# Kernel tuning notes

Hardware: AMD Instinct MI355X
Metric: run time of the kernel (lower is better)

## Reference

```python
import jax, jax.numpy as jnp
import numpy as np

D = 1024
H = 8
HD = D // H
SCALE = HD ** -0.5


def setup_inputs() -> dict:
    key = jax.random.key(0)
    ks = jax.random.split(key, 12)
    s = 0.02
    return {
        "x": jax.random.normal(ks[0], (4, 2048, D), dtype=jnp.float32),
        "attn_mask": jax.random.randint(ks[1], (2048, 2048), 0, 2, dtype=jnp.int32),
        "qkv_w": jax.random.normal(ks[2], (3 * D, D), dtype=jnp.float32) * s,
        "qkv_b": jnp.zeros((3 * D,), dtype=jnp.float32),
        "q_w": jax.random.normal(ks[3], (D, D), dtype=jnp.float32) * s,
        "q_b": jnp.zeros((D,), dtype=jnp.float32),
        "k_w": jax.random.normal(ks[4], (D, D), dtype=jnp.float32) * s,
        "k_b": jnp.zeros((D,), dtype=jnp.float32),
        "v_w": jax.random.normal(ks[5], (D, D), dtype=jnp.float32) * s,
        "v_b": jnp.zeros((D,), dtype=jnp.float32),
        "out_w": jax.random.normal(ks[6], (D, D), dtype=jnp.float32) * s,
        "out_b": jnp.zeros((D,), dtype=jnp.float32),
    }


def reference(x, attn_mask, qkv_w, qkv_b, q_w, q_b, k_w, k_b, v_w, v_b, out_w, out_b):
    B, S, _ = x.shape
    qkv = x @ qkv_w.T + qkv_b
    q, k, v = jnp.split(qkv, 3, axis=-1)
    # per-stream multi-head projections, then split heads: [B,H,S,HD]
    def heads(t, w, b):
        return (t @ w.T + b).reshape(B, S, H, HD).transpose(0, 2, 1, 3)
    q = heads(q, q_w, q_b)
    k = heads(k, k_w, k_b)
    v = heads(v, v_w, v_b)
    # scaled dot-product attention with masked softmax
    scores = jnp.einsum("bhqd,bhkd->bhqk", q, k) * SCALE
    scores = jnp.where(attn_mask == 1, -jnp.inf, scores)
    attn = jax.nn.softmax(scores, axis=-1)
    o = jnp.einsum("bhqk,bhkd->bhqd", attn, v)
    o = o.transpose(0, 2, 1, 3).reshape(B, S, D)
    return o @ out_w.T + out_b
```

## Files before the change

kernel.cpp:

```cpp
#include <hip/hip_runtime.h>
#include <stdint.h>

typedef unsigned short u16;
typedef unsigned int u32;
typedef unsigned long long u64;
using f32x4 = __attribute__((ext_vector_type(4))) float;
using s16x8 = __attribute__((ext_vector_type(8))) short;
using u16x4 = __attribute__((ext_vector_type(4))) unsigned short;

static constexpr float kQScale = (float)(0.08838834764831845 * 1.4426950408889634);

__device__ __forceinline__ u16 f2bf(float f) {
  uint32_t u = __float_as_uint(f);
  u += 0x7fffu + ((u >> 16) & 1u);
  return (u16)(u >> 16);
}

__device__ __forceinline__ float fexp2(float x) {
#if __has_builtin(__builtin_amdgcn_exp2f)
  return __builtin_amdgcn_exp2f(x);
#else
  return exp2f(x);
#endif
}

__device__ __forceinline__ void mfma16(f32x4& d, s16x8 a, s16x8 b) {
  asm volatile("v_mfma_f32_16x16x32_bf16 %0, %1, %2, %0" : "+v"(d) : "v"(a), "v"(b));
}
__device__ __forceinline__ f32x4 mfma16_z(s16x8 a, s16x8 b) {
  f32x4 d;
  asm volatile("v_mfma_f32_16x16x32_bf16 %0, %1, %2, 0" : "=&v"(d) : "v"(a), "v"(b));
  return d;
}

__device__ __forceinline__ void g2lds16(const void* g, void* l) {
  __builtin_amdgcn_global_load_lds(
      (__attribute__((address_space(1))) void*)(uintptr_t)g,
      (__attribute__((address_space(3))) void*)(uint32_t)(uintptr_t)l, 16, 0, 0);
}

__global__ __launch_bounds__(256) void cvt_f32_bf16(const float* __restrict__ in,
                                                    u16* __restrict__ out, int n) {
  int i = (blockIdx.x * 256 + threadIdx.x) * 4;
  if (i + 3 < n) {
    f32x4 v = *(const f32x4*)(in + i);
    u16x4 o = {f2bf(v.x), f2bf(v.y), f2bf(v.z), f2bf(v.w)};
    *(u16x4*)(out + i) = o;
  }
}

__global__ __launch_bounds__(256) void cvt4(const float* __restrict__ a, const float* __restrict__ b,
                                            const float* __restrict__ c, const float* __restrict__ d,
                                            u16* __restrict__ out) {
  int z = blockIdx.y;
  const float* in = z == 0 ? a : z == 1 ? b : z == 2 ? c : d;
  int i = (blockIdx.x * 256 + threadIdx.x) * 4;
  f32x4 v = *(const f32x4*)(in + i);
  u16x4 o = {f2bf(v.x), f2bf(v.y), f2bf(v.z), f2bf(v.w)};
  *(u16x4*)(out + (size_t)z * 1048576 + i) = o;
}

__global__ __launch_bounds__(256) void transpose_f32_bf16(const float* __restrict__ in,
                                                          u16* __restrict__ out, int R, int C) {
  __shared__ u16 tile[32][33];
  int bx = blockIdx.x, by = blockIdx.y;
  int tx = threadIdx.x & 31, ty = threadIdx.x >> 5;
#pragma unroll
  for (int k = 0; k < 4; ++k)
    tile[ty + k * 8][tx] = f2bf(in[(size_t)(by * 32 + ty + k * 8) * C + bx * 32 + tx]);
  __syncthreads();
#pragma unroll
  for (int k = 0; k < 4; ++k)
    out[(size_t)(bx * 32 + ty + k * 8) * R + by * 32 + tx] = tile[tx][ty + k * 8];
}

__global__ __launch_bounds__(256) void cbias3(const float* __restrict__ qw, const float* __restrict__ kw,
                                              const float* __restrict__ vw, const float* __restrict__ qkvb,
                                              const float* __restrict__ qb, const float* __restrict__ kb,
                                              const float* __restrict__ vb, float* __restrict__ out) {
  int z = blockIdx.y;
  const float* w = z == 0 ? qw : (z == 1 ? kw : vw);
  const float* ba = z == 0 ? qb : (z == 1 ? kb : vb);
  const float* bi = qkvb + z * 1024;
  int o = blockIdx.x * 4 + (threadIdx.x >> 6);
  int lane = threadIdx.x & 63;
  float s = 0.f;
  for (int m = lane; m < 1024; m += 64) s += w[o * 1024 + m] * bi[m];
#pragma unroll
  for (int d = 1; d < 64; d <<= 1) s += __shfl_xor(s, d);
  if (lane == 0) {
    float fin = s + ba[o];
    if (z == 0) fin *= kQScale;
    out[z * 1024 + o] = fin;
  }
}

__global__ __launch_bounds__(256) void pack_mask(const int* __restrict__ m, u64* __restrict__ pm) {
  int row = blockIdx.x;
  int wv = threadIdx.x >> 6, lane = threadIdx.x & 63;
#pragma unroll
  for (int i = 0; i < 8; ++i) {
    int word = wv * 8 + i;
    u64 b = __ballot(m[(size_t)row * 2048 + word * 64 + lane] == 1);
    if (lane == 0) pm[(size_t)row * 32 + word] = b;
  }
}

template <typename OUT_T, bool BIAS_PER_ROW>
__global__ __launch_bounds__(256, 2) void gemm_nt(const u16* __restrict__ A, int lda, long bsA,
                                                  const u16* __restrict__ B, int ldb, long bsB,
                                                  OUT_T* __restrict__ C, int ldc, long bsC,
                                                  const float* __restrict__ bias, long bsBias,
                                                  int NtilesN, int K, float scale_z0) {
  __shared__ __align__(16) u16 As[2 * 128 * 64];
  __shared__ __align__(16) u16 Bs[2 * 128 * 64];
  const int z = blockIdx.z;
  const float sc = (z == 0) ? scale_z0 : 1.f;
  A += (size_t)z * bsA; B += (size_t)z * bsB; C += (size_t)z * bsC;
  if (bias) bias += (size_t)z * bsBias;
  const int tm = blockIdx.x / NtilesN, tn = blockIdx.x % NtilesN;
  const int tid = threadIdx.x, lane = tid & 63, w = tid >> 6;
  const int wm = w >> 1, wn = w & 1;
  const int q = lane & 15, g = lane >> 4;
  f32x4 acc[4][4] = {};

  const u16* Ab = A + (size_t)(tm * 128 + (tid >> 3)) * lda + ((tid & 7) << 3);
  const u16* Bb = B + (size_t)(tn * 128 + (tid >> 3)) * ldb + ((tid & 7) << 3);

  auto stage = [&](int buf, int k0) {
    char* dA = (char*)As + buf * 16384 + (w << 10);
    char* dB = (char*)Bs + buf * 16384 + (w << 10);
#pragma unroll
    for (int it = 0; it < 4; ++it) {
      g2lds16(Ab + (size_t)(it * 32) * lda + k0, dA + it * 4096);
      g2lds16(Bb + (size_t)(it * 32) * ldb + k0, dB + it * 4096);
    }
  };

  const int nT = K >> 6;
  stage(0, 0);
  __syncthreads();
  for (int t = 0; t < nT; ++t) {
    if (t + 1 < nT) stage((t + 1) & 1, (t + 1) << 6);
    const char* AsR = (const char*)As + (t & 1) * 16384;
    const char* BsR = (const char*)Bs + (t & 1) * 16384;
#pragma unroll
    for (int kk = 0; kk < 2; ++kk) {
      s16x8 af[4], bf[4];
#pragma unroll
      for (int i = 0; i < 4; ++i)
        af[i] = *(const s16x8*)(AsR + (wm * 64 + i * 16 + q) * 128 + kk * 64 + g * 16);
#pragma unroll
      for (int i = 0; i < 4; ++i)
        bf[i] = *(const s16x8*)(BsR + (wn * 64 + i * 16 + q) * 128 + kk * 64 + g * 16);
#pragma unroll
      for (int mf = 0; mf < 4; ++mf)
#pragma unroll
        for (int nf = 0; nf < 4; ++nf) mfma16(acc[mf][nf], af[mf], bf[nf]);
    }
    __syncthreads();
  }
  asm volatile("s_nop 7\n\ts_nop 7");
#pragma unroll
  for (int mf = 0; mf < 4; ++mf)
#pragma unroll
    for (int nf = 0; nf < 4; ++nf) {
      const int row = tm * 128 + wm * 64 + mf * 16 + g * 4;
      const int col = tn * 128 + wn * 64 + nf * 16 + q;
      float bc = (!BIAS_PER_ROW && bias) ? bias[col] : 0.f;
#pragma unroll
      for (int r = 0; r < 4; ++r) {
        float v = acc[mf][nf][r] * sc;
        if (bias) v += BIAS_PER_ROW ? bias[row + r] : bc;
        if constexpr (sizeof(OUT_T) == 2)
          C[(size_t)(row + r) * ldc + col] = (OUT_T)f2bf(v);
        else
          C[(size_t)(row + r) * ldc + col] = (OUT_T)v;
      }
    }
}

__global__ __launch_bounds__(256, 2) void attn_fwd(const u16* __restrict__ Qb, const u16* __restrict__ Kb,
                                                   const u16* __restrict__ Vt, const u64* __restrict__ pmask,
                                                   u16* __restrict__ Ob) {
  __shared__ __align__(16) char K_lds[2 * 16384];
  __shared__ __align__(16) char V_lds[2 * 16384];
  __shared__ __align__(16) char P_lds[16384];
  const int n = blockIdx.x;
  const int slot = n >> 3;
  const int grp = (n & 7) * 4 + (slot >> 4);
  const int qt = slot & 15;
  const int h = grp & 7, b = grp >> 3;
  const int tid = threadIdx.x, w = tid >> 6, lane = tid & 63;
  const int q = lane & 15, g = lane >> 4;
  const int q0 = qt * 128;

  s16x8 qf[2][4];
#pragma unroll
  for (int m = 0; m < 2; ++m)
#pragma unroll
    for (int kk = 0; kk < 4; ++kk)
      qf[m][kk] = *(const s16x8*)(Qb + (size_t)(b * 2048 + q0 + w * 32 + m * 16 + q) * 1024 +
                                  h * 128 + kk * 32 + g * 8);

  f32x4 oacc[2][8] = {};
  float lp[2][4] = {};

  const int ksr = tid >> 4, ksc = tid & 15;
  const int vsr = tid >> 3, vsc = tid & 7;

  auto stageKV = [&](int buf, int s2) {
    const int kv0 = s2 * 64;
    char* kb = K_lds + buf * 16384 + (w << 10);
    char* vb = V_lds + buf * 16384 + (w << 10);
#pragma unroll
    for (int it = 0; it < 4; ++it) {
      int kr = it * 16 + ksr;
      g2lds16(Kb + (size_t)(b * 2048 + kv0 + kr) * 1024 + h * 128 + ((ksc ^ (kr & 7)) << 3),
              kb + it * 4096);
      int vr = it * 32 + vsr;
      g2lds16(Vt + (size_t)(h * 128 + vr) * 8192 + b * 2048 + kv0 + ((vsc ^ (vr & 7)) << 3),
              vb + it * 4096);
    }
  };

  stageKV(0, 0);
  __syncthreads();

  for (int s = 0; s < 32; ++s) {
    const int cur = s & 1;
    if (s + 1 < 32) stageKV(cur ^ 1, s + 1);
    const char* Kc = K_lds + cur * 16384;
    const char* Vc = V_lds + cur * 16384;

    u64 pw[2][4];
#pragma unroll
    for (int m = 0; m < 2; ++m)
#pragma unroll
      for (int r = 0; r < 4; ++r)
        pw[m][r] = pmask[(size_t)(q0 + w * 32 + m * 16 + g * 4 + r) * 32 + s];

    f32x4 sacc[2][4];
    __builtin_amdgcn_s_setprio(1);
#pragma unroll
    for (int kk = 0; kk < 4; ++kk) {
      s16x8 kf[4];
#pragma unroll
      for (int nn = 0; nn < 4; ++nn) {
        int kr = nn * 16 + q;
        kf[nn] = *(const s16x8*)(Kc + kr * 256 + ((((kk << 2) + g) ^ (kr & 7)) << 4));
      }
#pragma unroll
      for (int m = 0; m < 2; ++m)
#pragma unroll
        for (int nn = 0; nn < 4; ++nn) {
          if (kk == 0) sacc[m][nn] = mfma16_z(qf[m][0], kf[nn]);
          else         mfma16(sacc[m][nn], qf[m][kk], kf[nn]);
        }
    }
    __builtin_amdgcn_s_setprio(0);
    asm volatile("s_nop 7\n\ts_nop 7");

#pragma unroll
    for (int m = 0; m < 2; ++m)
#pragma unroll
      for (int r = 0; r < 4; ++r) {
        u32 lo = (u32)(pw[m][r] >> q);
        u32 hi = (u32)(pw[m][r] >> (32 + q));
#pragma unroll
        for (int nn = 0; nn < 4; ++nn) {
          u32 bit = (nn < 2) ? (lo >> (nn * 16)) : (hi >> ((nn - 2) * 16));
          float e = fexp2(sacc[nn == 0 ? m : m][nn][r] - 16.f);
          e = (bit & 1u) ? 0.f : e;
          sacc[m][nn][r] = e;
          lp[m][r] += e;
        }
      }

#pragma unroll
    for (int m = 0; m < 2; ++m)
#pragma unroll
      for (int r = 0; r < 4; ++r) {
        int row = w * 32 + m * 16 + g * 4 + r;
#pragma unroll
        for (int nn = 0; nn < 4; ++nn) {
          int colb = (nn * 16 + q) << 1;
          int byt = row * 128 + ((((colb >> 4) ^ (row & 7)) << 4) | (colb & 15));
          *(u16*)(P_lds + byt) = f2bf(sacc[m][nn][r]);
        }
      }

    __builtin_amdgcn_s_setprio(1);
#pragma unroll
    for (int kk = 0; kk < 2; ++kk) {
      s16x8 pf[2];
#pragma unroll
      for (int m = 0; m < 2; ++m) {
        int prow = w * 32 + m * 16 + q;
        pf[m] = *(const s16x8*)(P_lds + prow * 128 + ((((kk << 2) + g) ^ (prow & 7)) << 4));
      }
#pragma unroll
      for (int nd = 0; nd < 8; ++nd) {
        int dr = nd * 16 + q;
        s16x8 vf = *(const s16x8*)(Vc + dr * 128 + ((((kk << 2) + g) ^ (dr & 7)) << 4));
#pragma unroll
        for (int m = 0; m < 2; ++m) mfma16(oacc[m][nd], pf[m], vf);
      }
    }
    __builtin_amdgcn_s_setprio(0);
    __syncthreads();
  }

  asm volatile("s_nop 7\n\ts_nop 7");
  float rl[2][4];
#pragma unroll
  for (int m = 0; m < 2; ++m)
#pragma unroll
    for (int r = 0; r < 4; ++r) {
      float v = lp[m][r];
      v += __shfl_xor(v, 1); v += __shfl_xor(v, 2);
      v += __shfl_xor(v, 4); v += __shfl_xor(v, 8);
      rl[m][r] = 1.f / v;
    }
#pragma unroll
  for (int m = 0; m < 2; ++m)
#pragma unroll
    for (int nd = 0; nd < 8; ++nd)
#pragma unroll
      for (int r = 0; r < 4; ++r) {
        size_t trow = (size_t)(b * 2048 + q0 + w * 32 + m * 16 + g * 4 + r);
        Ob[trow * 1024 + h * 128 + nd * 16 + q] = f2bf(oacc[m][nd][r] * rl[m][r]);
      }
}

extern "C" void kernel_launch(void* const* d_in, const int* in_sizes, int n_in,
                              void* d_out, int out_size, void* d_ws, size_t ws_size,
                              hipStream_t stream) {
  (void)in_sizes; (void)n_in; (void)out_size; (void)ws_size;
  const float* x    = (const float*)d_in[0];
  const int*   am   = (const int*)d_in[1];
  const float* qkvw = (const float*)d_in[2];
  const float* qkvb = (const float*)d_in[3];
  const float* qw   = (const float*)d_in[4];
  const float* qb   = (const float*)d_in[5];
  const float* kw   = (const float*)d_in[6];
  const float* kb   = (const float*)d_in[7];
  const float* vw   = (const float*)d_in[8];
  const float* vb   = (const float*)d_in[9];
  const float* ow   = (const float*)d_in[10];
  const float* ob   = (const float*)d_in[11];

  char* p = (char*)d_ws;
  auto take = [&](size_t n) { char* r = p; p += (n + 255) & ~(size_t)255; return r; };
  u16* xb    = (u16*)take(8192ull * 1024 * 2);
  u16* qkvwT = (u16*)take(1024ull * 3072 * 2);
  u16* wb4   = (u16*)take(4ull * 1048576 * 2);
  u16* comb3 = (u16*)take(3ull * 1048576 * 2);
  float* cb3 = (float*)take(3ull * 1024 * 4);
  u16* QK2   = (u16*)take(2ull * 8192 * 1024 * 2);
  u16* V2t   = (u16*)take(8192ull * 1024 * 2);
  u64* pm    = (u64*)take(2048ull * 32 * 8);
  u16* Obuf  = xb;

  cvt_f32_bf16<<<8192, 256, 0, stream>>>(x, xb, 8192 * 1024);
  cvt4<<<dim3(1024, 4), 256, 0, stream>>>(qw, kw, vw, ow, wb4);
  transpose_f32_bf16<<<dim3(32, 96), 256, 0, stream>>>(qkvw, qkvwT, 3072, 1024);
  cbias3<<<dim3(256, 3), 256, 0, stream>>>(qw, kw, vw, qkvb, qb, kb, vb, cb3);

  gemm_nt<u16, false><<<dim3(64, 1, 3), 256, 0, stream>>>(
      wb4, 1024, 1048576, qkvwT, 3072, 1024, comb3, 1024, 1048576, nullptr, 0, 8, 1024, kQScale);
  gemm_nt<u16, false><<<dim3(512, 1, 2), 256, 0, stream>>>(
      xb, 1024, 0, comb3, 1024, 1048576, QK2, 1024, 8192ll * 1024, cb3, 1024, 8, 1024, 1.f);
  gemm_nt<u16, true><<<dim3(512, 1, 1), 256, 0, stream>>>(
      comb3 + 2 * 1048576, 1024, 0, xb, 1024, 0, V2t, 8192, 0, cb3 + 2048, 0, 64, 1024, 1.f);

  pack_mask<<<2048, 256, 0, stream>>>(am, pm);
  attn_fwd<<<512, 256, 0, stream>>>(QK2, QK2 + 8192ull * 1024, V2t, pm, Obuf);

  gemm_nt<float, false><<<dim3(512, 1, 1), 256, 0, stream>>>(
      Obuf, 1024, 0, wb4 + 3 * 1048576, 1024, 0, (float*)d_out, 1024, 0, ob, 0, 8, 1024, 1.f);
}
```

Baseline: 274.2 us.

## Use 32x32 MFMA in attention with in-register P and single-buffer GEMM LDS

The attention kernel moves from 16x16x32 to 32x32x16 bf16 MFMA and computes the transposed score tile, so each lane owns one query row. Softmax probabilities are packed to bf16 with v_cvt_pk and exchanged between wave halves through cross-lane shuffles, which removes the P round trip through LDS. The row-sum reduction is reduced to a single shuffle, and normalisation factors go through a small LDS table. Separately, the GEMM drops double-buffered LDS for a single buffer, which halves its shared memory but stops overlapping the next tile's load with compute.

```diff
diff --git a/kernel.cpp b/kernel.cpp
--- a/kernel.cpp
+++ b/kernel.cpp
@@ -5,8 +5,10 @@
 typedef unsigned int u32;
 typedef unsigned long long u64;
 using f32x4 = __attribute__((ext_vector_type(4))) float;
+using f32x16 = __attribute__((ext_vector_type(16))) float;
 using s16x8 = __attribute__((ext_vector_type(8))) short;
 using u16x4 = __attribute__((ext_vector_type(4))) unsigned short;
+using u32x4 = __attribute__((ext_vector_type(4))) u32;
 
 static constexpr float kQScale = (float)(0.08838834764831845 * 1.4426950408889634);
 
@@ -24,13 +26,17 @@
 #endif
 }
 
+__device__ __forceinline__ u32 cvtpk(float lo, float hi) {
+  u32 r;
+  asm("v_cvt_pk_bf16_f32 %0, %1, %2" : "=v"(r) : "v"(lo), "v"(hi));
+  return r;
+}
+
 __device__ __forceinline__ void mfma16(f32x4& d, s16x8 a, s16x8 b) {
   asm volatile("v_mfma_f32_16x16x32_bf16 %0, %1, %2, %0" : "+v"(d) : "v"(a), "v"(b));
 }
-__device__ __forceinline__ f32x4 mfma16_z(s16x8 a, s16x8 b) {
-  f32x4 d;
-  asm volatile("v_mfma_f32_16x16x32_bf16 %0, %1, %2, 0" : "=&v"(d) : "v"(a), "v"(b));
-  return d;
+__device__ __forceinline__ void mfma32(f32x16& d, s16x8 a, s16x8 b) {
+  asm volatile("v_mfma_f32_32x32x16_bf16 %0, %1, %2, %0" : "+v"(d) : "v"(a), "v"(b));
 }
 
 __device__ __forceinline__ void g2lds16(const void* g, void* l) {
@@ -112,8 +118,8 @@
                                                   OUT_T* __restrict__ C, int ldc, long bsC,
                                                   const float* __restrict__ bias, long bsBias,
                                                   int NtilesN, int K, float scale_z0) {
-  __shared__ __align__(16) u16 As[2 * 128 * 64];
-  __shared__ __align__(16) u16 Bs[2 * 128 * 64];
+  __shared__ __align__(16) u16 As[128 * 64];
+  __shared__ __align__(16) u16 Bs[128 * 64];
   const int z = blockIdx.z;
   const float sc = (z == 0) ? scale_z0 : 1.f;
   A += (size_t)z * bsA; B += (size_t)z * bsB; C += (size_t)z * bsC;
@@ -126,33 +132,25 @@
 
   const u16* Ab = A + (size_t)(tm * 128 + (tid >> 3)) * lda + ((tid & 7) << 3);
   const u16* Bb = B + (size_t)(tn * 128 + (tid >> 3)) * ldb + ((tid & 7) << 3);
-
-  auto stage = [&](int buf, int k0) {
-    char* dA = (char*)As + buf * 16384 + (w << 10);
-    char* dB = (char*)Bs + buf * 16384 + (w << 10);
+  char* AsW = (char*)As + (w << 10);
+  char* BsW = (char*)Bs + (w << 10);
+
+  for (int k0 = 0; k0 < K; k0 += 64) {
 #pragma unroll
     for (int it = 0; it < 4; ++it) {
-      g2lds16(Ab + (size_t)(it * 32) * lda + k0, dA + it * 4096);
-      g2lds16(Bb + (size_t)(it * 32) * ldb + k0, dB + it * 4096);
-    }
-  };
-
-  const int nT = K >> 6;
-  stage(0, 0);
-  __syncthreads();
-  for (int t = 0; t < nT; ++t) {
-    if (t + 1 < nT) stage((t + 1) & 1, (t + 1) << 6);
-    const char* AsR = (const char*)As + (t & 1) * 16384;
-    const char* BsR = (const char*)Bs + (t & 1) * 16384;
+      g2lds16(Ab + (size_t)(it * 32) * lda + k0, AsW + it * 4096);
+      g2lds16(Bb + (size_t)(it * 32) * ldb + k0, BsW + it * 4096);
+    }
+    __syncthreads();
 #pragma unroll
     for (int kk = 0; kk < 2; ++kk) {
       s16x8 af[4], bf[4];
 #pragma unroll
       for (int i = 0; i < 4; ++i)
-        af[i] = *(const s16x8*)(AsR + (wm * 64 + i * 16 + q) * 128 + kk * 64 + g * 16);
+        af[i] = *(const s16x8*)((const char*)As + (wm * 64 + i * 16 + q) * 128 + kk * 64 + g * 16);
 #pragma unroll
       for (int i = 0; i < 4; ++i)
-        bf[i] = *(const s16x8*)(BsR + (wn * 64 + i * 16 + q) * 128 + kk * 64 + g * 16);
+        bf[i] = *(const s16x8*)((const char*)Bs + (wn * 64 + i * 16 + q) * 128 + kk * 64 + g * 16);
 #pragma unroll
       for (int mf = 0; mf < 4; ++mf)
 #pragma unroll
@@ -185,29 +183,28 @@
                                                    u16* __restrict__ Ob) {
   __shared__ __align__(16) char K_lds[2 * 16384];
   __shared__ __align__(16) char V_lds[2 * 16384];
-  __shared__ __align__(16) char P_lds[16384];
+  __shared__ float l_red[4][32];
   const int n = blockIdx.x;
   const int slot = n >> 3;
   const int grp = (n & 7) * 4 + (slot >> 4);
   const int qt = slot & 15;
   const int h = grp & 7, b = grp >> 3;
   const int tid = threadIdx.x, w = tid >> 6, lane = tid & 63;
-  const int q = lane & 15, g = lane >> 4;
+  const int ql = lane & 31;
+  const int hi = lane >> 5;
   const int q0 = qt * 128;
 
-  s16x8 qf[2][4];
-#pragma unroll
-  for (int m = 0; m < 2; ++m)
-#pragma unroll
-    for (int kk = 0; kk < 4; ++kk)
-      qf[m][kk] = *(const s16x8*)(Qb + (size_t)(b * 2048 + q0 + w * 32 + m * 16 + q) * 1024 +
-                                  h * 128 + kk * 32 + g * 8);
-
-  f32x4 oacc[2][8] = {};
-  float lp[2][4] = {};
+  s16x8 qf[8];
+  const u16* qrow = Qb + (size_t)(b * 2048 + q0 + w * 32 + ql) * 1024 + h * 128 + 8 * hi;
+#pragma unroll
+  for (int kd = 0; kd < 8; ++kd) qf[kd] = *(const s16x8*)(qrow + 16 * kd);
+
+  f32x16 oacc[4] = {};
+  float lp = 0.f;
 
   const int ksr = tid >> 4, ksc = tid & 15;
   const int vsr = tid >> 3, vsc = tid & 7;
+  const int sw = ql & 15;
 
   auto stageKV = [&](int buf, int s2) {
     const int kv0 = s2 * 64;
@@ -216,7 +213,7 @@
 #pragma unroll
     for (int it = 0; it < 4; ++it) {
       int kr = it * 16 + ksr;
-      g2lds16(Kb + (size_t)(b * 2048 + kv0 + kr) * 1024 + h * 128 + ((ksc ^ (kr & 7)) << 3),
+      g2lds16(Kb + (size_t)(b * 2048 + kv0 + kr) * 1024 + h * 128 + ((ksc ^ (kr & 15)) << 3),
               kb + it * 4096);
       int vr = it * 32 + vsr;
       g2lds16(Vt + (size_t)(h * 128 + vr) * 8192 + b * 2048 + kv0 + ((vsc ^ (vr & 7)) << 3),
@@ -233,78 +230,66 @@
     const char* Kc = K_lds + cur * 16384;
     const char* Vc = V_lds + cur * 16384;
 
-    u64 pw[2][4];
-#pragma unroll
-    for (int m = 0; m < 2; ++m)
-#pragma unroll
-      for (int r = 0; r < 4; ++r)
-        pw[m][r] = pmask[(size_t)(q0 + w * 32 + m * 16 + g * 4 + r) * 32 + s];
-
-    f32x4 sacc[2][4];
+    u64 pw = pmask[(size_t)(q0 + w * 32 + ql) * 32 + s];
+
+    f32x16 sacc0 = {}, sacc1 = {};
     __builtin_amdgcn_s_setprio(1);
 #pragma unroll
-    for (int kk = 0; kk < 4; ++kk) {
-      s16x8 kf[4];
-#pragma unroll
-      for (int nn = 0; nn < 4; ++nn) {
-        int kr = nn * 16 + q;
-        kf[nn] = *(const s16x8*)(Kc + kr * 256 + ((((kk << 2) + g) ^ (kr & 7)) << 4));
-      }
-#pragma unroll
-      for (int m = 0; m < 2; ++m)
-#pragma unroll
-        for (int nn = 0; nn < 4; ++nn) {
-          if (kk == 0) sacc[m][nn] = mfma16_z(qf[m][0], kf[nn]);
-          else         mfma16(sacc[m][nn], qf[m][kk], kf[nn]);
-        }
+    for (int kd = 0; kd < 8; ++kd) {
+      int c = (2 * kd + hi) ^ sw;
+      s16x8 kf0 = *(const s16x8*)(Kc + ql * 256 + (c << 4));
+      s16x8 kf1 = *(const s16x8*)(Kc + (32 + ql) * 256 + (c << 4));
+      mfma32(sacc0, kf0, qf[kd]);
+      mfma32(sacc1, kf1, qf[kd]);
     }
     __builtin_amdgcn_s_setprio(0);
     asm volatile("s_nop 7\n\ts_nop 7");
 
-#pragma unroll
-    for (int m = 0; m < 2; ++m)
-#pragma unroll
-      for (int r = 0; r < 4; ++r) {
-        u32 lo = (u32)(pw[m][r] >> q);
-        u32 hi = (u32)(pw[m][r] >> (32 + q));
-#pragma unroll
-        for (int nn = 0; nn < 4; ++nn) {
-          u32 bit = (nn < 2) ? (lo >> (nn * 16)) : (hi >> ((nn - 2) * 16));
-          float e = fexp2(sacc[nn == 0 ? m : m][nn][r] - 16.f);
-          e = (bit & 1u) ? 0.f : e;
-          sacc[m][nn][r] = e;
-          lp[m][r] += e;
+    u32 Wp[8][2];
+#pragma unroll
+    for (int nt = 0; nt < 2; ++nt) {
+      u32 halfm = ((u32)(pw >> (32 * nt))) >> (4 * hi);
+#pragma unroll
+      for (int t = 0; t < 4; ++t) {
+        float e[4];
+#pragma unroll
+        for (int j = 0; j < 4; ++j) {
+          float ev = fexp2((nt == 0 ? sacc0[4 * t + j] : sacc1[4 * t + j]) - 16.f);
+          if ((halfm >> (8 * t + j)) & 1u) ev = 0.f;
+          e[j] = ev;
+          lp += ev;
         }
+        Wp[nt * 4 + t][0] = cvtpk(e[0], e[1]);
+        Wp[nt * 4 + t][1] = cvtpk(e[2], e[3]);
       }
-
-#pragma unroll
-    for (int m = 0; m < 2; ++m)
-#pragma unroll
-      for (int r = 0; r < 4; ++r) {
-        int row = w * 32 + m * 16 + g * 4 + r;
-#pragma unroll
-        for (int nn = 0; nn < 4; ++nn) {
-          int colb = (nn * 16 + q) << 1;
-          int byt = row * 128 + ((((colb >> 4) ^ (row & 7)) << 4) | (colb & 15));
-          *(u16*)(P_lds + byt) = f2bf(sacc[m][nn][r]);
-        }
-      }
+    }
+
+    s16x8 pa[4];
+#pragma unroll
+    for (int ks = 0; ks < 4; ++ks) {
+      u32 s0 = hi ? Wp[2 * ks][0] : Wp[2 * ks + 1][0];
+      u32 s1 = hi ? Wp[2 * ks][1] : Wp[2 * ks + 1][1];
+      u32 r0 = (u32)__shfl_xor((int)s0, 32);
+      u32 r1 = (u32)__shfl_xor((int)s1, 32);
+      u32 o0 = hi ? Wp[2 * ks + 1][0] : Wp[2 * ks][0];
+      u32 o1 = hi ? Wp[2 * ks + 1][1] : Wp[2 * ks][1];
+      u32x4 wv;
+      wv.x = hi ? r0 : o0;
+      wv.y = hi ? r1 : o1;
+      wv.z = hi ? o0 : r0;
+      wv.w = hi ? o1 : r1;
+      pa[ks] = __builtin_bit_cast(s16x8, wv);
+    }
+    asm volatile("s_nop 3");
 
     __builtin_amdgcn_s_setprio(1);
 #pragma unroll
-    for (int kk = 0; kk < 2; ++kk) {
-      s16x8 pf[2];
-#pragma unroll
-      for (int m = 0; m < 2; ++m) {
-        int prow = w * 32 + m * 16 + q;
-        pf[m] = *(const s16x8*)(P_lds + prow * 128 + ((((kk << 2) + g) ^ (prow & 7)) << 4));
-      }
-#pragma unroll
-      for (int nd = 0; nd < 8; ++nd) {
-        int dr = nd * 16 + q;
-        s16x8 vf = *(const s16x8*)(Vc + dr * 128 + ((((kk << 2) + g) ^ (dr & 7)) << 4));
-#pragma unroll
-        for (int m = 0; m < 2; ++m) mfma16(oacc[m][nd], pf[m], vf);
+    for (int ks = 0; ks < 4; ++ks) {
+#pragma unroll
+      for (int dt = 0; dt < 4; ++dt) {
+        int vrow = dt * 32 + ql;
+        s16x8 vf = *(const s16x8*)(Vc + vrow * 128 + ((((2 * ks + hi)) ^ (vrow & 7)) << 4));
+        mfma32(oacc[dt], pa[ks], vf);
       }
     }
     __builtin_amdgcn_s_setprio(0);
@@ -312,25 +297,20 @@
   }
 
   asm volatile("s_nop 7\n\ts_nop 7");
-  float rl[2][4];
-#pragma unroll
-  for (int m = 0; m < 2; ++m)
-#pragma unroll
-    for (int r = 0; r < 4; ++r) {
-      float v = lp[m][r];
-      v += __shfl_xor(v, 1); v += __shfl_xor(v, 2);
-      v += __shfl_xor(v, 4); v += __shfl_xor(v, 8);
-      rl[m][r] = 1.f / v;
-    }
-#pragma unroll
-  for (int m = 0; m < 2; ++m)
-#pragma unroll
-    for (int nd = 0; nd < 8; ++nd)
-#pragma unroll
-      for (int r = 0; r < 4; ++r) {
-        size_t trow = (size_t)(b * 2048 + q0 + w * 32 + m * 16 + g * 4 + r);
-        Ob[trow * 1024 + h * 128 + nd * 16 + q] = f2bf(oacc[m][nd][r] * rl[m][r]);
-      }
+  lp += __shfl_xor(lp, 32);
+  if (lane < 32) l_red[w][lane] = 1.f / lp;
+  float rl[16];
+#pragma unroll
+  for (int reg = 0; reg < 16; ++reg)
+    rl[reg] = l_red[w][(reg & 3) + 8 * (reg >> 2) + 4 * hi];
+#pragma unroll
+  for (int dt = 0; dt < 4; ++dt)
+#pragma unroll
+    for (int reg = 0; reg < 16; ++reg) {
+      int qr = (reg & 3) + 8 * (reg >> 2) + 4 * hi;
+      size_t trow = (size_t)(b * 2048 + q0 + w * 32 + qr);
+      Ob[trow * 1024 + h * 128 + dt * 32 + ql] = f2bf(oacc[dt][reg] * rl[reg]);
+    }
 }
 
 extern "C" void kernel_launch(void* const* d_in, const int* in_sizes, int n_in,
```

New measurement: 261.6 us. -4.6%, faster.
